# Kernel tuning notes

Hardware: AMD Instinct MI355X
Metric: run time of the kernel (lower is better)

The kernel has to match this reference:

```python
import jax, jax.numpy as jnp
import numpy as np

NL = 8      # num layers (['self','cross']*4)
H = 8       # heads
EPS = 1e-5  # torch LayerNorm default


def _layernorm(x, g, b):
    mu = jnp.mean(x, axis=-1, keepdims=True)
    var = jnp.mean((x - mu) ** 2, axis=-1, keepdims=True)
    return (x - mu) * jax.lax.rsqrt(var + EPS) * g + b


def _encoder_layer(x, source, Wq, Wk, Wv, Wm, W1, W2, g1, b1, g2, b2):
    # x: [N, L, C], source: [N, S, C]
    N, L, C = x.shape
    D = C // H
    q = (x @ Wq).reshape(N, L, H, D)
    k = (source @ Wk).reshape(N, -1, H, D)
    v = (source @ Wv).reshape(N, -1, H, D)
    # naive full attention: explicit [N, L, S, H] scores (as in FullAttention)
    qk = jnp.einsum('nlhd,nshd->nlsh', q, k)
    A = jax.nn.softmax(qk * (1.0 / np.sqrt(D)), axis=2)
    msg = jnp.einsum('nlsh,nshd->nlhd', A, v).reshape(N, L, C)
    msg = _layernorm(msg @ Wm, g1, b1)
    m = jnp.concatenate([x, msg], axis=-1)          # [N, L, 2C]
    m = jax.nn.relu(m @ W1) @ W2                    # [N, L, C]
    m = _layernorm(m, g2, b2)
    return x + m


def _loftr(feat0, feat1, Wq, Wk, Wv, Wm, W1, W2, g1, b1, g2, b2):
    names = ['self', 'cross'] * 4
    for i, name in enumerate(names):
        p = (Wq[i], Wk[i], Wv[i], Wm[i], W1[i], W2[i], g1[i], b1[i], g2[i], b2[i])
        if name == 'self':
            feat0 = _encoder_layer(feat0, feat0, *p)
            feat1 = _encoder_layer(feat1, feat1, *p)
        else:  # cross; note feat0 is updated before being fed to feat1's layer
            feat0 = _encoder_layer(feat0, feat1, *p)
            feat1 = _encoder_layer(feat1, feat0, *p)
    return jnp.stack([feat0, feat1], axis=0)  # [2, N, L, C]


def setup_inputs() -> dict:
    key = jax.random.key(0)
    ks = jax.random.split(key, 10)
    N, L, C = 8, 1024, 768
    s = 1.0 / np.sqrt(C)       # xavier-ish scale for [C, C]
    s2 = 1.0 / np.sqrt(2 * C)  # for MLP fan-in 2C
    return {
        'feat0': jax.random.normal(ks[0], (N, L, C), jnp.float32),
        'feat1': jax.random.normal(ks[1], (N, L, C), jnp.float32),
        'Wq': jax.random.normal(ks[2], (NL, C, C), jnp.float32) * s,
        'Wk': jax.random.normal(ks[3], (NL, C, C), jnp.float32) * s,
        'Wv': jax.random.normal(ks[4], (NL, C, C), jnp.float32) * s,
        'Wm': jax.random.normal(ks[5], (NL, C, C), jnp.float32) * s,
        'W1': jax.random.normal(ks[6], (NL, 2 * C, 2 * C), jnp.float32) * s2,
        'W2': jax.random.normal(ks[7], (NL, 2 * C, C), jnp.float32) * s2,
        'g1': jnp.ones((NL, C), jnp.float32),
        'b1': jnp.zeros((NL, C), jnp.float32),
        'g2': jnp.ones((NL, C), jnp.float32),
        'b2': jnp.zeros((NL, C), jnp.float32),
    }


def reference(feat0, feat1, Wq, Wk, Wv, Wm, W1, W2, g1, b1, g2, b2):
    return _loftr(feat0, feat1, Wq, Wk, Wv, Wm, W1, W2, g1, b1, g2, b2)
```

## Files before the change

kernel.cpp:

```cpp
#include <hip/hip_runtime.h>
#include <hip/hip_bf16.h>

typedef __hip_bfloat16 bf16;
typedef __bf16 bf16x8 __attribute__((ext_vector_type(8)));
typedef float f32x4 __attribute__((ext_vector_type(4)));

#define AS1 __attribute__((address_space(1)))
#define AS3 __attribute__((address_space(3)))
__device__ __forceinline__ void gl_lds16(const void* g, void* l) {
    __builtin_amdgcn_global_load_lds((const AS1 void*)g, (AS3 void*)l, 16, 0, 0);
}

__device__ __forceinline__ float fexp2(float x) {
#if __has_builtin(__builtin_amdgcn_exp2f)
    return __builtin_amdgcn_exp2f(x);
#else
    return exp2f(x);
#endif
}

__device__ __forceinline__ int xcd_swz(int did, int nwg) {
    return (did & 7) * (nwg >> 3) + (did >> 3);
}


__global__ __launch_bounds__(256) void cvt_f32_bf16_k(const float* __restrict__ in, bf16* __restrict__ out,
                                                      int ostride, int total)
{
    int i = blockIdx.x * 256 + threadIdx.x;
    int e = i * 4;
    if (e >= total) return;
    int row = e / 768;
    int col = e - row * 768;
    const float4 f = *(const float4*)(in + e);
    bf16 o4[4];
    o4[0] = __float2bfloat16(f.x); o4[1] = __float2bfloat16(f.y);
    o4[2] = __float2bfloat16(f.z); o4[3] = __float2bfloat16(f.w);
    *(uint2*)(out + (size_t)row * ostride + col) = *(uint2*)o4;
}

__global__ void transpose_cvt_k(const float* __restrict__ in, bf16* __restrict__ out, int R, int C,
                                float scale, size_t lstride)
{
    __shared__ float t[32][33];
    const int tx = threadIdx.x, ty = threadIdx.y;
    in  += (size_t)blockIdx.z * R * C;
    out += (size_t)blockIdx.z * lstride;
    const int c0 = blockIdx.x * 32, r0 = blockIdx.y * 32;
    #pragma unroll
    for (int i = 0; i < 4; ++i)
        t[ty + i*8][tx] = in[(size_t)(r0 + ty + i*8) * C + c0 + tx];
    __syncthreads();
    #pragma unroll
    for (int i = 0; i < 4; ++i)
        out[(size_t)(c0 + ty + i*8) * R + r0 + tx] = __float2bfloat16(t[tx][ty + i*8] * scale);
}

template<int EPI>
__global__ __launch_bounds__(256) void gemm_bt_k(const bf16* __restrict__ A, int lda,
                                                 const bf16* __restrict__ BT, int K,
                                                 void* __restrict__ Cp, int ldc, int colshift,
                                                 bf16* __restrict__ Ck, bf16* __restrict__ Cv)
{
    __shared__ bf16 a_sm[3][4096];
    __shared__ bf16 b_sm[3][4096];
    const int tid = threadIdx.x;
    const int lane = tid & 63;
    const int wid = tid >> 6;
    const int wr = wid >> 1, wc = wid & 1;

    const int nwg = gridDim.x * gridDim.y;
    const int did = blockIdx.x + gridDim.x * blockIdx.y;
    const int wgid = xcd_swz(did, nwg);
    const int col0 = (wgid % gridDim.y) * 128;
    const int row0 = (wgid / gridDim.y) * 128;
    const int g = lane >> 4, r16 = lane & 15;

    const int r4 = lane >> 2;
    const int sc = (lane & 3) ^ ((lane >> 3) & 3);
    const bf16* gA[2]; const bf16* gB[2]; int loff[2];
    #pragma unroll
    for (int i = 0; i < 2; ++i) {
        const int blk = wid*2 + i;
        gA[i] = A  + (size_t)(row0 + blk*16 + r4) * lda + sc*8;
        gB[i] = BT + (size_t)(col0 + blk*16 + r4) * K   + sc*8;
        loff[i] = blk * 512;
    }
    const int foff = r16*32 + ((g ^ ((r16 >> 1) & 3)) * 8);

    f32x4 acc[4][4];
    #pragma unroll
    for (int m = 0; m < 4; ++m)
        #pragma unroll
        for (int n = 0; n < 4; ++n)
            #pragma unroll
            for (int r = 0; r < 4; ++r) acc[m][n][r] = 0.f;

    #pragma unroll
    for (int i = 0; i < 2; ++i) {
        gl_lds16(gA[i],      &a_sm[0][loff[i]]);
        gl_lds16(gB[i],      &b_sm[0][loff[i]]);
    }
    #pragma unroll
    for (int i = 0; i < 2; ++i) {
        gl_lds16(gA[i] + 32, &a_sm[1][loff[i]]);
        gl_lds16(gB[i] + 32, &b_sm[1][loff[i]]);
    }

    int cur = 0, pre = 2;
    for (int k0 = 0; k0 < K; k0 += 32) {
        if (k0 + 32 < K) asm volatile("s_waitcnt vmcnt(4)" ::: "memory");
        else             asm volatile("s_waitcnt vmcnt(0)" ::: "memory");
        __builtin_amdgcn_s_barrier();
        if (k0 + 64 < K) {
            #pragma unroll
            for (int i = 0; i < 2; ++i) {
                gl_lds16(gA[i] + k0 + 64, &a_sm[pre][loff[i]]);
                gl_lds16(gB[i] + k0 + 64, &b_sm[pre][loff[i]]);
            }
        }
        bf16x8 af[4], bfr[4];
        #pragma unroll
        for (int m = 0; m < 4; ++m) af[m]  = *(const bf16x8*)&a_sm[cur][(wr*4 + m)*512 + foff];
        #pragma unroll
        for (int n = 0; n < 4; ++n) bfr[n] = *(const bf16x8*)&b_sm[cur][(wc*4 + n)*512 + foff];
        asm volatile("s_waitcnt lgkmcnt(0)" ::: "memory");
        __builtin_amdgcn_s_setprio(1);
        #pragma unroll
        for (int m = 0; m < 4; ++m)
            #pragma unroll
            for (int n = 0; n < 4; ++n)
                acc[m][n] = __builtin_amdgcn_mfma_f32_16x16x32_bf16(af[m], bfr[n], acc[m][n], 0, 0, 0);
        __builtin_amdgcn_s_setprio(0);
        cur = (cur == 2) ? 0 : cur + 1;
        pre = (pre == 2) ? 0 : pre + 1;
    }

    #pragma unroll
    for (int m = 0; m < 4; ++m) {
        const int orow = row0 + wr*64 + m*16 + g*4;
        #pragma unroll
        for (int n = 0; n < 4; ++n) {
            const int ocol = col0 + wc*64 + n*16 + r16;
            if (EPI == 4 || EPI == 5) {
                const int ce = ocol + colshift;
                const int seg = ce / 768;
                const int ci = ce - seg*768;
                if (seg <= 1) {
                    bf16* dst = (seg == 0) ? (bf16*)Cp : Ck;
                    #pragma unroll
                    for (int r = 0; r < 4; ++r)
                        dst[(size_t)(orow + r)*768 + ci] = __float2bfloat16(acc[m][n][r]);
                } else {
                    const int nn = orow >> 10, ss = orow & 1023;
                    const int hh = ci / 96, dd = ci - hh * 96;
                    bf16 pk[4];
                    #pragma unroll
                    for (int r = 0; r < 4; ++r) pk[r] = __float2bfloat16(acc[m][n][r]);
                    *(uint2*)&Cv[(((size_t)nn*8 + hh)*96 + dd)*1024 + ss] = *(uint2*)pk;
                }
            } else {
                #pragma unroll
                for (int r = 0; r < 4; ++r) {
                    float v = acc[m][n][r];
                    if (EPI == 1) v = fmaxf(v, 0.f);
                    if (EPI == 2) ((float*)Cp)[(size_t)(orow + r)*ldc + ocol] = v;
                    else          ((bf16*)Cp) [(size_t)(orow + r)*ldc + ocol] = __float2bfloat16(v);
                }
            }
        }
    }
}

__global__ __launch_bounds__(512) void attn_k(const bf16* __restrict__ qb, const bf16* __restrict__ kb,
                                              const bf16* __restrict__ vtb, bf16* __restrict__ msgb)
{
    __shared__ bf16 kv_sm[3][12*512];
    __shared__ bf16 p_sm_all[8][32][40];
    const int tid = threadIdx.x;
    const int lane = tid & 63;
    const int w = tid >> 6;
    const int g = lane >> 4, r16 = lane & 15;

    const int nwg = gridDim.x * gridDim.y;
    const int did = blockIdx.x + gridDim.x * blockIdx.y;
    const int wgid = xcd_swz(did, nwg);
    const int qx = wgid % gridDim.x;
    const int nh = wgid / gridDim.x;
    const int n = nh >> 3, h = nh & 7;
    const int q0 = qx * 256 + w * 32;

    bf16 (*p_sm)[40] = p_sm_all[w];

    const bf16* kbase = kb  + ((size_t)n*1024)*768 + (size_t)h*96;
    const bf16* vbase = vtb + ((size_t)(n*8 + h))*96*1024;

    bf16x8 aq[2][3];
    #pragma unroll
    for (int qh = 0; qh < 2; ++qh) {
        const size_t qoff = ((size_t)n*1024 + q0 + qh*16 + r16) * 768 + (size_t)h*96;
        #pragma unroll
        for (int c = 0; c < 3; ++c) aq[qh][c] = *(const bf16x8*)&qb[qoff + c*32 + g*8];
    }

    const int r4 = lane >> 2;
    const int sc = (lane & 3) ^ ((lane >> 3) & 3);
    const bf16* gsrc[2]; size_t gstep[2]; int dstoff[2];
    const int nissue = (w < 4) ? 2 : 1;
    #pragma unroll
    for (int jj = 0; jj < 2; ++jj) {
        const int issue = w + jj*8;
        if (issue < 6) {
            const int c = issue >> 1, kh = issue & 1;
            gsrc[jj]  = kbase + (size_t)(kh*16 + r4)*768 + c*32 + sc*8;
            gstep[jj] = 768;
        } else {
            gsrc[jj]  = vbase + (size_t)((issue-6)*16 + r4)*1024 + sc*8;
            gstep[jj] = 1;
        }
        dstoff[jj] = (issue < 12) ? issue * 512 : 0;
    }
    const int foff = r16*32 + ((g ^ ((r16 >> 1) & 3)) * 8);

    float m_run[2], l_run[2];
    #pragma unroll
    for (int qh = 0; qh < 2; ++qh) { m_run[qh] = -1e30f; l_run[qh] = 0.f; }
    f32x4 o[2][6];
    #pragma unroll
    for (int qg = 0; qg < 2; ++qg)
        #pragma unroll
        for (int f = 0; f < 6; ++f)
            #pragma unroll
            for (int r = 0; r < 4; ++r) o[qg][f][r] = 0.f;

    gl_lds16(gsrc[0], &kv_sm[0][dstoff[0]]);
    if (nissue == 2) gl_lds16(gsrc[1], &kv_sm[0][dstoff[1]]);
    gl_lds16(gsrc[0] + 32 * gstep[0], &kv_sm[1][dstoff[0]]);
    if (nissue == 2) gl_lds16(gsrc[1] + 32 * gstep[1], &kv_sm[1][dstoff[1]]);

    int cur = 0, pre = 2;
    for (int kt = 0; kt < 1024; kt += 32) {
        if (kt + 32 < 1024) {
            if (nissue == 2) asm volatile("s_waitcnt vmcnt(2)" ::: "memory");
            else             asm volatile("s_waitcnt vmcnt(1)" ::: "memory");
        } else {
            asm volatile("s_waitcnt vmcnt(0)" ::: "memory");
        }
        __builtin_amdgcn_s_barrier();
        if (kt + 64 < 1024) {
            gl_lds16(gsrc[0] + (size_t)(kt + 64) * gstep[0], &kv_sm[pre][dstoff[0]]);
            if (nissue == 2) gl_lds16(gsrc[1] + (size_t)(kt + 64) * gstep[1], &kv_sm[pre][dstoff[1]]);
        }
        const bf16* rd = kv_sm[cur];

        f32x4 s[2][2];
        #pragma unroll
        for (int kh = 0; kh < 2; ++kh)
            #pragma unroll
            for (int qh = 0; qh < 2; ++qh)
                #pragma unroll
                for (int r = 0; r < 4; ++r) s[kh][qh][r] = 0.f;
        __builtin_amdgcn_s_setprio(1);
        #pragma unroll
        for (int c = 0; c < 3; ++c) {
            bf16x8 ak0 = *(const bf16x8*)&rd[(c*2 + 0)*512 + foff];
            bf16x8 ak1 = *(const bf16x8*)&rd[(c*2 + 1)*512 + foff];
            s[0][0] = __builtin_amdgcn_mfma_f32_16x16x32_bf16(ak0, aq[0][c], s[0][0], 0, 0, 0);
            s[0][1] = __builtin_amdgcn_mfma_f32_16x16x32_bf16(ak0, aq[1][c], s[0][1], 0, 0, 0);
            s[1][0] = __builtin_amdgcn_mfma_f32_16x16x32_bf16(ak1, aq[0][c], s[1][0], 0, 0, 0);
            s[1][1] = __builtin_amdgcn_mfma_f32_16x16x32_bf16(ak1, aq[1][c], s[1][1], 0, 0, 0);
        }
        __builtin_amdgcn_s_setprio(0);

        float pmv[2], gr[2];
        #pragma unroll
        for (int qh = 0; qh < 2; ++qh) {
            float pm = fmaxf(fmaxf(fmaxf(s[0][qh][0], s[0][qh][1]), fmaxf(s[0][qh][2], s[0][qh][3])),
                             fmaxf(fmaxf(s[1][qh][0], s[1][qh][1]), fmaxf(s[1][qh][2], s[1][qh][3])));
            pm = fmaxf(pm, __shfl_xor(pm, 16, 64));
            pm = fmaxf(pm, __shfl_xor(pm, 32, 64));
            pmv[qh] = pm;
            gr[qh] = pm - m_run[qh];
        }
        if (__any(fmaxf(gr[0], gr[1]) > 8.0f)) {
            float alpha_c[2];
            #pragma unroll
            for (int qh = 0; qh < 2; ++qh) {
                float mn = fmaxf(m_run[qh], pmv[qh]);
                alpha_c[qh] = fexp2(m_run[qh] - mn);
                m_run[qh] = mn;
                l_run[qh] *= alpha_c[qh];
            }
            #pragma unroll
            for (int qg = 0; qg < 2; ++qg)
                #pragma unroll
                for (int r = 0; r < 4; ++r) {
                    float ar = __shfl(alpha_c[qg], g*4 + r, 64);
                    #pragma unroll
                    for (int f = 0; f < 6; ++f) o[qg][f][r] *= ar;
                }
        }
        #pragma unroll
        for (int qh = 0; qh < 2; ++qh) {
            bf16 pk0[4], pk1[4];
            float rs = 0.f;
            #pragma unroll
            for (int r = 0; r < 4; ++r) {
                float p0 = fexp2(s[0][qh][r] - m_run[qh]);
                float p1 = fexp2(s[1][qh][r] - m_run[qh]);
                rs += p0 + p1;
                pk0[r] = __float2bfloat16(p0);
                pk1[r] = __float2bfloat16(p1);
            }
            rs += __shfl_xor(rs, 16, 64);
            rs += __shfl_xor(rs, 32, 64);
            l_run[qh] += rs;
            *(uint2*)&p_sm[qh*16 + r16][g*4]      = *(uint2*)pk0;
            *(uint2*)&p_sm[qh*16 + r16][16 + g*4] = *(uint2*)pk1;
        }

        bf16x8 pa0 = *(const bf16x8*)&p_sm[r16][g*8];
        bf16x8 pa1 = *(const bf16x8*)&p_sm[16 + r16][g*8];
        __builtin_amdgcn_s_setprio(1);
        #pragma unroll
        for (int f = 0; f < 6; ++f) {
            bf16x8 bv = *(const bf16x8*)&rd[(6 + f)*512 + foff];
            o[0][f] = __builtin_amdgcn_mfma_f32_16x16x32_bf16(pa0, bv, o[0][f], 0, 0, 0);
            o[1][f] = __builtin_amdgcn_mfma_f32_16x16x32_bf16(pa1, bv, o[1][f], 0, 0, 0);
        }
        __builtin_amdgcn_s_setprio(0);
        asm volatile("s_waitcnt lgkmcnt(0)" ::: "memory");
        cur = (cur == 2) ? 0 : cur + 1;
        pre = (pre == 2) ? 0 : pre + 1;
    }

    float linv[2][4];
    #pragma unroll
    for (int qg = 0; qg < 2; ++qg)
        #pragma unroll
        for (int r = 0; r < 4; ++r)
            linv[qg][r] = 1.0f / __shfl(l_run[qg], g*4 + r, 64);

    #pragma unroll
    for (int qg = 0; qg < 2; ++qg) {
        const size_t obase = ((size_t)n*1024 + q0 + qg*16 + g*4) * 768 + (size_t)h*96;
        #pragma unroll
        for (int f = 0; f < 6; ++f)
            #pragma unroll
            for (int r = 0; r < 4; ++r)
                msgb[obase + (size_t)r*768 + f*16 + r16] = __float2bfloat16(o[qg][f][r] * linv[qg][r]);
    }
}

template<int MODE>
__global__ __launch_bounds__(256) void ln_k(const float* __restrict__ in, const float* __restrict__ g,
                                            const float* __restrict__ b, bf16* __restrict__ outc,
                                            float* __restrict__ x)
{
    const int row = blockIdx.x;
    const int tid = threadIdx.x;
    const float* rp = in + (size_t)row * 768;
    float v[3];
    #pragma unroll
    for (int j = 0; j < 3; ++j) v[j] = rp[tid + j*256];
    float s  = v[0] + v[1] + v[2];
    float sq = v[0]*v[0] + v[1]*v[1] + v[2]*v[2];
    #pragma unroll
    for (int off = 32; off >= 1; off >>= 1) {
        s  += __shfl_xor(s,  off, 64);
        sq += __shfl_xor(sq, off, 64);
    }
    __shared__ float red[2][4];
    const int wid = tid >> 6;
    if ((tid & 63) == 0) { red[0][wid] = s; red[1][wid] = sq; }
    __syncthreads();
    const float S  = red[0][0] + red[0][1] + red[0][2] + red[0][3];
    const float SQ = red[1][0] + red[1][1] + red[1][2] + red[1][3];
    const float mu = S * (1.f/768.f);
    float var = SQ * (1.f/768.f) - mu*mu;
    var = fmaxf(var, 0.f);
    const float rs = rsqrtf(var + 1e-5f);
    #pragma unroll
    for (int j = 0; j < 3; ++j) {
        const int c = tid + j*256;
        const float y = (v[j] - mu) * rs * g[c] + b[c];
        if (MODE == 1) {
            outc[(size_t)row*1536 + 768 + c] = __float2bfloat16(y);
        } else {
            const float nx = x[(size_t)row*768 + c] + y;
            x[(size_t)row*768 + c] = nx;
            outc[(size_t)row*1536 + c] = __float2bfloat16(nx);
        }
    }
}

extern "C" void kernel_launch(void* const* d_in, const int* in_sizes, int n_in,
                              void* d_out, int out_size, void* d_ws, size_t ws_size,
                              hipStream_t stream)
{
    const float* feat0 = (const float*)d_in[0];
    const float* feat1 = (const float*)d_in[1];
    const float* Wq = (const float*)d_in[2];
    const float* Wk = (const float*)d_in[3];
    const float* Wv = (const float*)d_in[4];
    const float* Wm = (const float*)d_in[5];
    const float* W1 = (const float*)d_in[6];
    const float* W2 = (const float*)d_in[7];
    const float* g1 = (const float*)d_in[8];
    const float* b1 = (const float*)d_in[9];
    const float* g2 = (const float*)d_in[10];
    const float* b2 = (const float*)d_in[11];

    char* p = (char*)d_ws;
    auto take = [&](size_t bytes) { char* q = p; p += (bytes + 255) & ~(size_t)255; return q; };
    bf16* wqkvT = (bf16*)take((size_t)8*2304*768*2);
    bf16* wmT = (bf16*)take((size_t)8*768*768*2);
    bf16* w1T = (bf16*)take((size_t)8*1536*1536*2);
    bf16* w2T = (bf16*)take((size_t)8*768*1536*2);
    bf16* concat0 = (bf16*)take((size_t)8192*1536*2);
    bf16* concat1 = (bf16*)take((size_t)8192*1536*2);
    bf16* qb   = (bf16*)take((size_t)8192*768*2);
    bf16* kb   = (bf16*)take((size_t)8192*768*2);
    bf16* vtb  = (bf16*)take((size_t)8192*768*2);
    bf16* m1b  = (bf16*)take((size_t)8192*1536*2);
    float* t0  = (float*)take((size_t)8192*768*4);
    bf16* msgb = qb;

    float* x0 = (float*)d_out;
    float* x1 = x0 + (size_t)8192*768;

    hipMemcpyAsync(x0, feat0, (size_t)8192*768*4, hipMemcpyDeviceToDevice, stream);
    hipMemcpyAsync(x1, feat1, (size_t)8192*768*4, hipMemcpyDeviceToDevice, stream);

    const float s_qk = 0.14724444f;
    const dim3 tb(32, 8);
    const size_t QKV = (size_t)2304*768;
    transpose_cvt_k<<<dim3(24,24,8), tb, 0, stream>>>(Wq, wqkvT,            768, 768,  s_qk, QKV);
    transpose_cvt_k<<<dim3(24,24,8), tb, 0, stream>>>(Wk, wqkvT + 768*768,  768, 768,  1.0f, QKV);
    transpose_cvt_k<<<dim3(24,24,8), tb, 0, stream>>>(Wv, wqkvT + 1536*768, 768, 768,  1.0f, QKV);
    transpose_cvt_k<<<dim3(24,24,8), tb, 0, stream>>>(Wm, wmT, 768, 768,  1.0f, (size_t)768*768);
    transpose_cvt_k<<<dim3(48,48,8), tb, 0, stream>>>(W1, w1T, 1536, 1536, 1.0f, (size_t)1536*1536);
    transpose_cvt_k<<<dim3(24,48,8), tb, 0, stream>>>(W2, w2T, 1536, 768,  1.0f, (size_t)1536*768);

    const int total = 8192*768;
    cvt_f32_bf16_k<<<6144, 256, 0, stream>>>(feat0, concat0, 1536, total);
    cvt_f32_bf16_k<<<6144, 256, 0, stream>>>(feat1, concat1, 1536, total);

    auto encode = [&](float* x, bf16* cS, const bf16* cR, int i, bool self) {
        const bf16* wl = wqkvT + (size_t)i * QKV;
        if (self) {
            gemm_bt_k<4><<<dim3(64,18), 256, 0, stream>>>(cS, 1536, wl, 768, qb, 768, 0, kb, vtb);
        } else {
            gemm_bt_k<0><<<dim3(64,6),  256, 0, stream>>>(cS, 1536, wl, 768, qb, 768, 0, nullptr, nullptr);
            gemm_bt_k<5><<<dim3(64,12), 256, 0, stream>>>(cR, 1536, wl + (size_t)768*768, 768,
                                                          nullptr, 0, 768, kb, vtb);
        }
        attn_k<<<dim3(4,64), 512, 0, stream>>>(qb, kb, vtb, msgb);
        gemm_bt_k<2><<<dim3(64,6),  256, 0, stream>>>(msgb, 768, wmT + (size_t)i*768*768, 768,
                                                      t0, 768, 0, nullptr, nullptr);
        ln_k<1><<<8192, 256, 0, stream>>>(t0, g1 + i*768, b1 + i*768, cS, nullptr);
        gemm_bt_k<1><<<dim3(64,12), 256, 0, stream>>>(cS, 1536, w1T + (size_t)i*1536*1536, 1536,
                                                      m1b, 1536, 0, nullptr, nullptr);
        gemm_bt_k<2><<<dim3(64,6),  256, 0, stream>>>(m1b, 1536, w2T + (size_t)i*768*1536, 1536,
                                                      t0, 768, 0, nullptr, nullptr);
        ln_k<2><<<8192, 256, 0, stream>>>(t0, g2 + i*768, b2 + i*768, cS, x);
    };

    for (int i = 0; i < 8; ++i) {
        if ((i & 1) == 0) { encode(x0, concat0, concat0, i, true);  encode(x1, concat1, concat1, i, true); }
        else              { encode(x0, concat0, concat1, i, false); encode(x1, concat1, concat0, i, false); }
    }
}
```

Baseline: 3.809 ms.

## Batch self-attention layers across both features and store pre-LayerNorm outputs in bf16

When the workspace is large enough, each self layer runs once with M=16384 rows over both feature streams. This relies on concat0/concat1 and x0/x1 sitting next to each other in memory, and it doubles the grid sizes so the GPU is better filled while halving the number of launches. The Wm and W2 GEMM outputs that feed LayerNorm are now written as bf16 instead of fp32, which cuts write and read traffic. The cost is that the LayerNorm inputs are rounded to bf16, and the batched path only runs if ws_size allows it.

```diff
diff --git a/kernel.cpp b/kernel.cpp
--- a/kernel.cpp
+++ b/kernel.cpp
@@ -164,8 +164,7 @@
                 for (int r = 0; r < 4; ++r) {
                     float v = acc[m][n][r];
                     if (EPI == 1) v = fmaxf(v, 0.f);
-                    if (EPI == 2) ((float*)Cp)[(size_t)(orow + r)*ldc + ocol] = v;
-                    else          ((bf16*)Cp) [(size_t)(orow + r)*ldc + ocol] = __float2bfloat16(v);
+                    ((bf16*)Cp)[(size_t)(orow + r)*ldc + ocol] = __float2bfloat16(v);
                 }
             }
         }
@@ -353,16 +352,16 @@
 }
 
 template<int MODE>
-__global__ __launch_bounds__(256) void ln_k(const float* __restrict__ in, const float* __restrict__ g,
+__global__ __launch_bounds__(256) void ln_k(const bf16* __restrict__ in, const float* __restrict__ g,
                                             const float* __restrict__ b, bf16* __restrict__ outc,
                                             float* __restrict__ x)
 {
     const int row = blockIdx.x;
     const int tid = threadIdx.x;
-    const float* rp = in + (size_t)row * 768;
+    const bf16* rp = in + (size_t)row * 768;
     float v[3];
     #pragma unroll
-    for (int j = 0; j < 3; ++j) v[j] = rp[tid + j*256];
+    for (int j = 0; j < 3; ++j) v[j] = __bfloat162float(rp[tid + j*256]);
     float s  = v[0] + v[1] + v[2];
     float sq = v[0]*v[0] + v[1]*v[1] + v[2]*v[2];
     #pragma unroll
@@ -411,19 +410,25 @@
     const float* g2 = (const float*)d_in[10];
     const float* b2 = (const float*)d_in[11];
 
-    char* p = (char*)d_ws;
-    auto take = [&](size_t bytes) { char* q = p; p += (bytes + 255) & ~(size_t)255; return q; };
-    bf16* wqkvT = (bf16*)take((size_t)8*2304*768*2);
-    bf16* wmT = (bf16*)take((size_t)8*768*768*2);
-    bf16* w1T = (bf16*)take((size_t)8*1536*1536*2);
-    bf16* w2T = (bf16*)take((size_t)8*768*1536*2);
-    bf16* concat0 = (bf16*)take((size_t)8192*1536*2);
-    bf16* concat1 = (bf16*)take((size_t)8192*1536*2);
-    bf16* qb   = (bf16*)take((size_t)8192*768*2);
-    bf16* kb   = (bf16*)take((size_t)8192*768*2);
-    bf16* vtb  = (bf16*)take((size_t)8192*768*2);
-    bf16* m1b  = (bf16*)take((size_t)8192*1536*2);
-    float* t0  = (float*)take((size_t)8192*768*4);
+    bf16 *wqkvT, *wmT, *w1T, *w2T, *concat0, *concat1, *qb, *kb, *vtb, *m1b, *t0b;
+    auto plan = [&](int RB) -> size_t {
+        char* p = (char*)d_ws;
+        auto take = [&](size_t bytes) { char* q = p; p += (bytes + 255) & ~(size_t)255; return q; };
+        wqkvT = (bf16*)take((size_t)8*2304*768*2);
+        wmT  = (bf16*)take((size_t)8*768*768*2);
+        w1T  = (bf16*)take((size_t)8*1536*1536*2);
+        w2T  = (bf16*)take((size_t)8*768*1536*2);
+        concat0 = (bf16*)take((size_t)8192*1536*2);
+        concat1 = (bf16*)take((size_t)8192*1536*2);
+        qb   = (bf16*)take((size_t)RB*768*2);
+        kb   = (bf16*)take((size_t)RB*768*2);
+        vtb  = (bf16*)take((size_t)RB*768*2);
+        m1b  = (bf16*)take((size_t)RB*1536*2);
+        t0b  = (bf16*)take((size_t)RB*768*2);
+        return (size_t)(p - (char*)d_ws);
+    };
+    bool batched = plan(16384) <= ws_size;
+    if (!batched) plan(8192);
     bf16* msgb = qb;
 
     float* x0 = (float*)d_out;
@@ -446,28 +451,38 @@
     cvt_f32_bf16_k<<<6144, 256, 0, stream>>>(feat0, concat0, 1536, total);
     cvt_f32_bf16_k<<<6144, 256, 0, stream>>>(feat1, concat1, 1536, total);
 
-    auto encode = [&](float* x, bf16* cS, const bf16* cR, int i, bool self) {
+    auto encode = [&](float* x, bf16* cS, const bf16* cR, int i, bool self, int M) {
         const bf16* wl = wqkvT + (size_t)i * QKV;
+        const int MT = M / 128;
         if (self) {
-            gemm_bt_k<4><<<dim3(64,18), 256, 0, stream>>>(cS, 1536, wl, 768, qb, 768, 0, kb, vtb);
+            gemm_bt_k<4><<<dim3(MT,18), 256, 0, stream>>>(cS, 1536, wl, 768, qb, 768, 0, kb, vtb);
         } else {
-            gemm_bt_k<0><<<dim3(64,6),  256, 0, stream>>>(cS, 1536, wl, 768, qb, 768, 0, nullptr, nullptr);
-            gemm_bt_k<5><<<dim3(64,12), 256, 0, stream>>>(cR, 1536, wl + (size_t)768*768, 768,
+            gemm_bt_k<0><<<dim3(MT,6),  256, 0, stream>>>(cS, 1536, wl, 768, qb, 768, 0, nullptr, nullptr);
+            gemm_bt_k<5><<<dim3(MT,12), 256, 0, stream>>>(cR, 1536, wl + (size_t)768*768, 768,
                                                           nullptr, 0, 768, kb, vtb);
         }
-        attn_k<<<dim3(4,64), 512, 0, stream>>>(qb, kb, vtb, msgb);
-        gemm_bt_k<2><<<dim3(64,6),  256, 0, stream>>>(msgb, 768, wmT + (size_t)i*768*768, 768,
-                                                      t0, 768, 0, nullptr, nullptr);
-        ln_k<1><<<8192, 256, 0, stream>>>(t0, g1 + i*768, b1 + i*768, cS, nullptr);
-        gemm_bt_k<1><<<dim3(64,12), 256, 0, stream>>>(cS, 1536, w1T + (size_t)i*1536*1536, 1536,
+        attn_k<<<dim3(4, (M/1024)*8), 512, 0, stream>>>(qb, kb, vtb, msgb);
+        gemm_bt_k<0><<<dim3(MT,6),  256, 0, stream>>>(msgb, 768, wmT + (size_t)i*768*768, 768,
+                                                      t0b, 768, 0, nullptr, nullptr);
+        ln_k<1><<<M, 256, 0, stream>>>(t0b, g1 + i*768, b1 + i*768, cS, nullptr);
+        gemm_bt_k<1><<<dim3(MT,12), 256, 0, stream>>>(cS, 1536, w1T + (size_t)i*1536*1536, 1536,
                                                       m1b, 1536, 0, nullptr, nullptr);
-        gemm_bt_k<2><<<dim3(64,6),  256, 0, stream>>>(m1b, 1536, w2T + (size_t)i*768*1536, 1536,
-                                                      t0, 768, 0, nullptr, nullptr);
-        ln_k<2><<<8192, 256, 0, stream>>>(t0, g2 + i*768, b2 + i*768, cS, x);
+        gemm_bt_k<0><<<dim3(MT,6),  256, 0, stream>>>(m1b, 1536, w2T + (size_t)i*768*1536, 1536,
+                                                      t0b, 768, 0, nullptr, nullptr);
+        ln_k<2><<<M, 256, 0, stream>>>(t0b, g2 + i*768, b2 + i*768, cS, x);
     };
 
     for (int i = 0; i < 8; ++i) {
-        if ((i & 1) == 0) { encode(x0, concat0, concat0, i, true);  encode(x1, concat1, concat1, i, true); }
-        else              { encode(x0, concat0, concat1, i, false); encode(x1, concat1, concat0, i, false); }
-    }
-}
+        if ((i & 1) == 0) {
+            if (batched) {
+                encode(x0, concat0, concat0, i, true, 16384);
+            } else {
+                encode(x0, concat0, concat0, i, true, 8192);
+                encode(x1, concat1, concat1, i, true, 8192);
+            }
+        } else {
+            encode(x0, concat0, concat1, i, false, 8192);
+            encode(x1, concat1, concat0, i, false, 8192);
+        }
+    }
+}
```

New measurement: 3.440 ms. 1.11x faster.
